# Performance work log

Hardware: AMD Instinct MI355X
Metric: run time of the kernel (lower is better)

The kernel has to match this reference:

```python
import jax, jax.numpy as jnp
import numpy as np

N_NODES = 50000
N_EDGES = 600000
D = 128
THETA = (0.5, -1.0, 0.5)  # len(theta) must be 3 to match learnable_diag[3, in_feats]


def setup_inputs() -> dict:
    key = jax.random.key(0)
    k1, k2, k3, k4, k5 = jax.random.split(key, 5)
    feat = jax.random.normal(k1, (N_NODES, D), dtype=jnp.float32)
    edge_index = jax.random.randint(k2, (2, N_EDGES), 0, N_NODES)  # [src; dst]
    # learnable_diag = torch.rand(3, in_feats)
    diag = jax.random.uniform(k3, (3, D), dtype=jnp.float32)
    # nn.Linear(out_feats, out_feats) with xavier_uniform weight, zero bias
    limit = float(np.sqrt(6.0 / (D + D)))
    W = jax.random.uniform(k4, (D, D), dtype=jnp.float32, minval=-limit, maxval=limit)
    b = jnp.zeros((D,), dtype=jnp.float32)
    return {"feat": feat, "edge_index": edge_index, "diag": diag, "W": W, "b": b}


def reference(feat, edge_index, diag, W, b):
    src, dst = edge_index[0], edge_index[1]
    n = feat.shape[0]
    # in_degrees: count of incoming edges per node
    deg = jax.ops.segment_sum(jnp.ones_like(dst, dtype=feat.dtype), dst, num_segments=n)
    d_invsqrt = jnp.clip(deg, 1.0, None) ** -0.5  # [N]
    d_invsqrt = d_invsqrt[:, None]  # [N,1]

    h = (THETA[0] * feat) * diag[0]
    h = h @ W.T + b  # nn.Linear

    for k in range(1, len(THETA)):
        # unnLaplacian: feat - (A @ (feat * Dinv)) * Dinv * diag[k]
        msg = feat * d_invsqrt  # [N,D]
        agg = jax.ops.segment_sum(msg[src], dst, num_segments=n)  # SpMM: copy_u + sum
        feat = feat - agg * d_invsqrt * diag[k]
        h = h + THETA[k] * feat
    return h
```

## Files before the change

kernel.cpp:

```cpp
#include <hip/hip_runtime.h>

#define NN 50000
#define NE 600000
#define D  128
#define NBLK 196

typedef __attribute__((ext_vector_type(8))) short bf16x8;
typedef __attribute__((ext_vector_type(4))) float floatx4;

__device__ __forceinline__ unsigned short bf16_rne(float f) {
    union { float f; unsigned u; } v; v.f = f;
    unsigned r = v.u + 0x7FFFu + ((v.u >> 16) & 1u);
    return (unsigned short)(r >> 16);
}
__device__ __forceinline__ unsigned pack2(float a, float b) {
    return (unsigned)bf16_rne(a) | ((unsigned)bf16_rne(b) << 16);
}

__global__ __launch_bounds__(256) void prep_kernel(const float* __restrict__ W,
                                                   const float* __restrict__ diag,
                                                   unsigned short* __restrict__ Wb,
                                                   int* __restrict__ deg_i,
                                                   unsigned int* __restrict__ zrow0,
                                                   unsigned int* __restrict__ zrow1) {
    int g = blockIdx.x * 256 + threadIdx.x;
    if (g < NN) deg_i[g] = 0;
    if (g < 16384) {
        int j = g & 127;
        Wb[g] = bf16_rne(0.5f * diag[j] * W[g]);
    }
    if (g < 64) { zrow0[g] = 0u; zrow1[g] = 0u; }
}

__global__ __launch_bounds__(256) void hist_kernel(const int* __restrict__ dst,
                                                   int* __restrict__ deg_i) {
    int e = blockIdx.x * 256 + threadIdx.x;
    if (e < NE) atomicAdd(&deg_i[dst[e]], 1);
}

__global__ __launch_bounds__(256) void scan1_kernel(const int* __restrict__ deg_i,
                                                    int* __restrict__ row_ptr,
                                                    int* __restrict__ partials,
                                                    float* __restrict__ dinvf,
                                                    float* __restrict__ rdegf) {
    __shared__ int sh[256];
    int i = blockIdx.x * 256 + threadIdx.x;
    int dg = (i < NN) ? deg_i[i] : 0;
    if (i < NN) {
        float d = (float)dg;
        float dc = d > 1.0f ? d : 1.0f;
        dinvf[i] = rsqrtf(dc);
        rdegf[i] = sqrtf(dc);
    }
    sh[threadIdx.x] = dg;
    __syncthreads();
    #pragma unroll
    for (int off = 1; off < 256; off <<= 1) {
        int t = (threadIdx.x >= off) ? sh[threadIdx.x - off] : 0;
        __syncthreads();
        sh[threadIdx.x] += t;
        __syncthreads();
    }
    if (i < NN) row_ptr[i + 1] = sh[threadIdx.x];
    if (threadIdx.x == 255) partials[blockIdx.x] = sh[255];
}

__global__ __launch_bounds__(256) void scan2_kernel(int* __restrict__ partials) {
    __shared__ int sh[256];
    sh[threadIdx.x] = (threadIdx.x < NBLK) ? partials[threadIdx.x] : 0;
    __syncthreads();
    #pragma unroll
    for (int off = 1; off < 256; off <<= 1) {
        int t = (threadIdx.x >= off) ? sh[threadIdx.x - off] : 0;
        __syncthreads();
        sh[threadIdx.x] += t;
        __syncthreads();
    }
    if (threadIdx.x < NBLK) partials[threadIdx.x] = sh[threadIdx.x];
}

__global__ __launch_bounds__(256) void scan3_kernel(int* __restrict__ row_ptr,
                                                    const int* __restrict__ partials,
                                                    int* __restrict__ fillc) {
    int i = blockIdx.x * 256 + threadIdx.x;
    if (i < NN) {
        int add = (blockIdx.x > 0) ? partials[blockIdx.x - 1] : 0;
        row_ptr[i + 1] += add;
        fillc[i] = 0;
    }
    if (i == 0) row_ptr[0] = 0;
}

__global__ __launch_bounds__(256) void fill_kernel(const int* __restrict__ src,
                                                   const int* __restrict__ dst,
                                                   const int* __restrict__ row_ptr,
                                                   int* __restrict__ fillc,
                                                   int* __restrict__ csr) {
    int e = blockIdx.x * 256 + threadIdx.x;
    if (e < NE) {
        int t = dst[e];
        int pos = row_ptr[t] + atomicAdd(&fillc[t], 1);
        csr[pos] = src[e];
    }
}

__global__ __launch_bounds__(256) void gemm_mfma_kernel(const float* __restrict__ feat,
                                                        const unsigned short* __restrict__ Wb,
                                                        const float* __restrict__ b,
                                                        const float* __restrict__ dinvf,
                                                        unsigned short* __restrict__ featb_s,
                                                        float* __restrict__ out) {
    const int wv   = threadIdx.x >> 6;
    const int lane = threadIdx.x & 63;
    const int r16  = lane & 15;
    const int quad = lane >> 4;
    const int m0   = blockIdx.x * 64 + wv * 16;

    const int mrow = m0 + r16;
    const int mc   = (mrow < NN) ? mrow : (NN - 1);
    const float* arow = feat + (size_t)mc * D + quad * 8;
    const float di = dinvf[mc];

    bf16x8 afrag[4];
    #pragma unroll
    for (int kc = 0; kc < 4; ++kc) {
        const float4 f0 = *(const float4*)(arow + kc * 32);
        const float4 f1 = *(const float4*)(arow + kc * 32 + 4);
        bf16x8 a;
        a[0] = (short)bf16_rne(f0.x); a[1] = (short)bf16_rne(f0.y);
        a[2] = (short)bf16_rne(f0.z); a[3] = (short)bf16_rne(f0.w);
        a[4] = (short)bf16_rne(f1.x); a[5] = (short)bf16_rne(f1.y);
        a[6] = (short)bf16_rne(f1.z); a[7] = (short)bf16_rne(f1.w);
        afrag[kc] = a;
        if (mrow < NN) {
            uint4 st;
            st.x = pack2(f0.x * di, f0.y * di);
            st.y = pack2(f0.z * di, f0.w * di);
            st.z = pack2(f1.x * di, f1.y * di);
            st.w = pack2(f1.z * di, f1.w * di);
            *(uint4*)(featb_s + (size_t)mc * D + quad * 8 + kc * 32) = st;
        }
    }

    floatx4 acc[8];
    #pragma unroll
    for (int nt = 0; nt < 8; ++nt) acc[nt] = (floatx4)(0.0f);

    #pragma unroll
    for (int nt = 0; nt < 8; ++nt) {
        const unsigned short* brow = Wb + (size_t)(nt * 16 + r16) * D + quad * 8;
        #pragma unroll
        for (int kc = 0; kc < 4; ++kc) {
            const bf16x8 bfrag = *(const bf16x8*)(brow + kc * 32);
            acc[nt] = __builtin_amdgcn_mfma_f32_16x16x32_bf16(afrag[kc], bfrag, acc[nt], 0, 0, 0);
        }
    }

    #pragma unroll
    for (int nt = 0; nt < 8; ++nt) {
        const int d = nt * 16 + r16;
        const float bd = b[d];
        #pragma unroll
        for (int r = 0; r < 4; ++r) {
            const int i = m0 + quad * 4 + r;
            if (i < NN) out[(size_t)i * D + d] = acc[nt][r] + bd;
        }
    }
}

__device__ __forceinline__ float2 gather_acc(const unsigned short* __restrict__ rows,
                                             const int* __restrict__ csr,
                                             int e0, int e1, int lane) {
    float2 acc = make_float2(0.0f, 0.0f);
    for (int bse = e0; bse < e1; bse += 64) {
        int idx = bse + lane;
        int s = (idx < e1) ? csr[idx] : NN;
        int cnt8 = (min(64, e1 - bse) + 7) & ~7;
        for (int k = 0; k < cnt8; k += 8) {
            #pragma unroll
            for (int u = 0; u < 8; ++u) {
                int ss = __shfl(s, k + u);
                unsigned pv = *(const unsigned*)(rows + (size_t)ss * D + 2 * lane);
                acc.x += __uint_as_float(pv << 16);
                acc.y += __uint_as_float(pv & 0xFFFF0000u);
            }
        }
    }
    return acc;
}

__global__ __launch_bounds__(256) void gather1_kernel(const unsigned short* __restrict__ featb_s,
                                                      const int* __restrict__ csr,
                                                      const int* __restrict__ row_ptr,
                                                      const float* __restrict__ dinvf,
                                                      const float* __restrict__ diag,
                                                      const float* __restrict__ feat0,
                                                      unsigned int* __restrict__ feat1s) {
    const int node = blockIdx.x * 4 + (threadIdx.x >> 6);
    const int lane = threadIdx.x & 63;
    float2 acc = gather_acc(featb_s, csr, row_ptr[node], row_ptr[node + 1], lane);

    const size_t o2 = (size_t)node * (D / 2) + lane;
    const float di = dinvf[node];
    const float2 bs = *(const float2*)&feat0[2 * o2];
    const float2 dg = *(const float2*)&diag[D + 2 * lane];
    float rx = bs.x - acc.x * di * dg.x;
    float ry = bs.y - acc.y * di * dg.y;
    feat1s[o2] = pack2(rx * di, ry * di);
}

__global__ __launch_bounds__(256) void gather2_kernel(const unsigned short* __restrict__ feat1s,
                                                      const int* __restrict__ csr,
                                                      const int* __restrict__ row_ptr,
                                                      const float* __restrict__ dinvf,
                                                      const float* __restrict__ rdegf,
                                                      const float* __restrict__ diag,
                                                      float* __restrict__ outp) {
    const int node = blockIdx.x * 4 + (threadIdx.x >> 6);
    const int lane = threadIdx.x & 63;
    float2 acc = gather_acc(feat1s, csr, row_ptr[node], row_ptr[node + 1], lane);

    const size_t o2 = (size_t)node * (D / 2) + lane;
    const float di = dinvf[node];
    const float rd = rdegf[node];
    const unsigned bp = ((const unsigned*)feat1s)[o2];
    const float2 dg = *(const float2*)&diag[2 * D + 2 * lane];
    float bx = __uint_as_float(bp << 16) * rd;
    float by = __uint_as_float(bp & 0xFFFF0000u) * rd;
    float2 cur = *(const float2*)&outp[2 * o2];
    cur.x -= 0.5f * (bx + acc.x * di * dg.x);
    cur.y -= 0.5f * (by + acc.y * di * dg.y);
    *(float2*)&outp[2 * o2] = cur;
}

extern "C" void kernel_launch(void* const* d_in, const int* in_sizes, int n_in,
                              void* d_out, int out_size, void* d_ws, size_t ws_size,
                              hipStream_t stream) {
    const float* feat = (const float*)d_in[0];
    const int*   eidx = (const int*)d_in[1];
    const float* diag = (const float*)d_in[2];
    const float* W    = (const float*)d_in[3];
    const float* b    = (const float*)d_in[4];
    float* out = (float*)d_out;

    const int* src = eidx;
    const int* dst = eidx + NE;

    unsigned short* featb_s = (unsigned short*)d_ws;
    unsigned short* feat1s  = featb_s + (size_t)(NN + 1) * D;
    int*   csr      = (int*)(feat1s + (size_t)(NN + 1) * D);
    float* dinvf    = (float*)(csr + NE);
    float* rdegf    = dinvf + NN;
    int*   deg_i    = (int*)(rdegf + NN);
    int*   row_ptr  = deg_i + NN;
    int*   fillc    = row_ptr + NN + 2;
    int*   partials = fillc + NN;
    unsigned short* Wb = (unsigned short*)(partials + 256);

    prep_kernel<<<NBLK, 256, 0, stream>>>(W, diag, Wb, deg_i,
                                          (unsigned int*)(featb_s + (size_t)NN * D),
                                          (unsigned int*)(feat1s + (size_t)NN * D));

    hist_kernel<<<(NE + 255) / 256, 256, 0, stream>>>(dst, deg_i);
    scan1_kernel<<<NBLK, 256, 0, stream>>>(deg_i, row_ptr, partials, dinvf, rdegf);
    scan2_kernel<<<1, 256, 0, stream>>>(partials);
    scan3_kernel<<<NBLK, 256, 0, stream>>>(row_ptr, partials, fillc);
    fill_kernel<<<(NE + 255) / 256, 256, 0, stream>>>(src, dst, row_ptr, fillc, csr);

    gemm_mfma_kernel<<<(NN + 63) / 64, 256, 0, stream>>>(feat, Wb, b, dinvf, featb_s, out);

    gather1_kernel<<<NN / 4, 256, 0, stream>>>(featb_s, csr, row_ptr, dinvf, diag,
                                               feat, (unsigned int*)feat1s);
    gather2_kernel<<<NN / 4, 256, 0, stream>>>(feat1s, csr, row_ptr, dinvf, rdegf, diag, out);
}
```

Before: 229.4 us.

## Fuse CSR build stages into one cooperative kernel with grid syncs

Merges the prep, histogram, three scan stages and CSR fill into a single cooperative kernel of 784 blocks, with grid-wide syncs between phases. The aim is to cut the launch overhead and inter-kernel gaps of six small launches. In exchange each phase runs on a fixed grid with grid-stride loops. Grid sync barriers carry their own cost and can limit occupancy.

```diff
diff --git a/kernel.cpp b/kernel.cpp
--- a/kernel.cpp
+++ b/kernel.cpp
@@ -1,9 +1,13 @@
 #include <hip/hip_runtime.h>
+#include <hip/hip_cooperative_groups.h>
+
+namespace cg = cooperative_groups;
 
 #define NN 50000
 #define NE 600000
 #define D  128
 #define NBLK 196
+#define CGRID 784
 
 typedef __attribute__((ext_vector_type(8))) short bf16x8;
 typedef __attribute__((ext_vector_type(4))) float floatx4;
@@ -17,89 +21,84 @@
     return (unsigned)bf16_rne(a) | ((unsigned)bf16_rne(b) << 16);
 }
 
-__global__ __launch_bounds__(256) void prep_kernel(const float* __restrict__ W,
-                                                   const float* __restrict__ diag,
-                                                   unsigned short* __restrict__ Wb,
-                                                   int* __restrict__ deg_i,
-                                                   unsigned int* __restrict__ zrow0,
-                                                   unsigned int* __restrict__ zrow1) {
-    int g = blockIdx.x * 256 + threadIdx.x;
+__global__ __launch_bounds__(256) void build_kernel(const int* __restrict__ src,
+                                                    const int* __restrict__ dst,
+                                                    const float* __restrict__ W,
+                                                    const float* __restrict__ diag,
+                                                    unsigned short* __restrict__ Wb,
+                                                    int* __restrict__ deg_i,
+                                                    int* __restrict__ row_ptr,
+                                                    int* __restrict__ fillc,
+                                                    int* __restrict__ partials,
+                                                    float* __restrict__ dinvf,
+                                                    float* __restrict__ rdegf,
+                                                    int* __restrict__ csr,
+                                                    unsigned int* __restrict__ zrow0,
+                                                    unsigned int* __restrict__ zrow1) {
+    cg::grid_group grid = cg::this_grid();
+    __shared__ int sh[256];
+    const int t = threadIdx.x;
+    const int b = blockIdx.x;
+    const int g = b * 256 + t;
+    const int G = CGRID * 256;
+
     if (g < NN) deg_i[g] = 0;
     if (g < 16384) {
         int j = g & 127;
         Wb[g] = bf16_rne(0.5f * diag[j] * W[g]);
     }
     if (g < 64) { zrow0[g] = 0u; zrow1[g] = 0u; }
-}
-
-__global__ __launch_bounds__(256) void hist_kernel(const int* __restrict__ dst,
-                                                   int* __restrict__ deg_i) {
-    int e = blockIdx.x * 256 + threadIdx.x;
-    if (e < NE) atomicAdd(&deg_i[dst[e]], 1);
-}
-
-__global__ __launch_bounds__(256) void scan1_kernel(const int* __restrict__ deg_i,
-                                                    int* __restrict__ row_ptr,
-                                                    int* __restrict__ partials,
-                                                    float* __restrict__ dinvf,
-                                                    float* __restrict__ rdegf) {
-    __shared__ int sh[256];
-    int i = blockIdx.x * 256 + threadIdx.x;
-    int dg = (i < NN) ? deg_i[i] : 0;
-    if (i < NN) {
-        float d = (float)dg;
-        float dc = d > 1.0f ? d : 1.0f;
-        dinvf[i] = rsqrtf(dc);
-        rdegf[i] = sqrtf(dc);
-    }
-    sh[threadIdx.x] = dg;
-    __syncthreads();
-    #pragma unroll
-    for (int off = 1; off < 256; off <<= 1) {
-        int t = (threadIdx.x >= off) ? sh[threadIdx.x - off] : 0;
+    grid.sync();
+
+    for (int e = g; e < NE; e += G) atomicAdd(&deg_i[dst[e]], 1);
+    grid.sync();
+
+    if (b < NBLK) {
+        int i = b * 256 + t;
+        int dg = (i < NN) ? deg_i[i] : 0;
+        if (i < NN) {
+            float d = (float)dg;
+            float dc = d > 1.0f ? d : 1.0f;
+            dinvf[i] = rsqrtf(dc);
+            rdegf[i] = sqrtf(dc);
+        }
+        sh[t] = dg;
         __syncthreads();
-        sh[threadIdx.x] += t;
+        #pragma unroll
+        for (int off = 1; off < 256; off <<= 1) {
+            int v = (t >= off) ? sh[t - off] : 0;
+            __syncthreads();
+            sh[t] += v;
+            __syncthreads();
+        }
+        if (i < NN) row_ptr[i + 1] = sh[t];
+        if (t == 255) partials[b] = sh[255];
+    }
+    grid.sync();
+
+    if (b < NBLK) {
+        sh[t] = (t < NBLK) ? partials[t] : 0;
         __syncthreads();
-    }
-    if (i < NN) row_ptr[i + 1] = sh[threadIdx.x];
-    if (threadIdx.x == 255) partials[blockIdx.x] = sh[255];
-}
-
-__global__ __launch_bounds__(256) void scan2_kernel(int* __restrict__ partials) {
-    __shared__ int sh[256];
-    sh[threadIdx.x] = (threadIdx.x < NBLK) ? partials[threadIdx.x] : 0;
-    __syncthreads();
-    #pragma unroll
-    for (int off = 1; off < 256; off <<= 1) {
-        int t = (threadIdx.x >= off) ? sh[threadIdx.x - off] : 0;
-        __syncthreads();
-        sh[threadIdx.x] += t;
-        __syncthreads();
-    }
-    if (threadIdx.x < NBLK) partials[threadIdx.x] = sh[threadIdx.x];
-}
-
-__global__ __launch_bounds__(256) void scan3_kernel(int* __restrict__ row_ptr,
-                                                    const int* __restrict__ partials,
-                                                    int* __restrict__ fillc) {
-    int i = blockIdx.x * 256 + threadIdx.x;
-    if (i < NN) {
-        int add = (blockIdx.x > 0) ? partials[blockIdx.x - 1] : 0;
-        row_ptr[i + 1] += add;
-        fillc[i] = 0;
-    }
-    if (i == 0) row_ptr[0] = 0;
-}
-
-__global__ __launch_bounds__(256) void fill_kernel(const int* __restrict__ src,
-                                                   const int* __restrict__ dst,
-                                                   const int* __restrict__ row_ptr,
-                                                   int* __restrict__ fillc,
-                                                   int* __restrict__ csr) {
-    int e = blockIdx.x * 256 + threadIdx.x;
-    if (e < NE) {
-        int t = dst[e];
-        int pos = row_ptr[t] + atomicAdd(&fillc[t], 1);
+        #pragma unroll
+        for (int off = 1; off < 256; off <<= 1) {
+            int v = (t >= off) ? sh[t - off] : 0;
+            __syncthreads();
+            sh[t] += v;
+            __syncthreads();
+        }
+        int add = (b > 0) ? sh[b - 1] : 0;
+        int i = b * 256 + t;
+        if (i < NN) {
+            row_ptr[i + 1] += add;
+            fillc[i] = 0;
+        }
+        if (g == 0) row_ptr[0] = 0;
+    }
+    grid.sync();
+
+    for (int e = g; e < NE; e += G) {
+        int tt = dst[e];
+        int pos = row_ptr[tt] + atomicAdd(&fillc[tt], 1);
         csr[pos] = src[e];
     }
 }
@@ -257,15 +256,19 @@
     int*   partials = fillc + NN;
     unsigned short* Wb = (unsigned short*)(partials + 256);
 
-    prep_kernel<<<NBLK, 256, 0, stream>>>(W, diag, Wb, deg_i,
-                                          (unsigned int*)(featb_s + (size_t)NN * D),
-                                          (unsigned int*)(feat1s + (size_t)NN * D));
-
-    hist_kernel<<<(NE + 255) / 256, 256, 0, stream>>>(dst, deg_i);
-    scan1_kernel<<<NBLK, 256, 0, stream>>>(deg_i, row_ptr, partials, dinvf, rdegf);
-    scan2_kernel<<<1, 256, 0, stream>>>(partials);
-    scan3_kernel<<<NBLK, 256, 0, stream>>>(row_ptr, partials, fillc);
-    fill_kernel<<<(NE + 255) / 256, 256, 0, stream>>>(src, dst, row_ptr, fillc, csr);
+    unsigned int* zrow0 = (unsigned int*)(featb_s + (size_t)NN * D);
+    unsigned int* zrow1 = (unsigned int*)(feat1s + (size_t)NN * D);
+
+    {
+        void* args[] = {
+            (void*)&src, (void*)&dst, (void*)&W, (void*)&diag,
+            (void*)&Wb, (void*)&deg_i, (void*)&row_ptr, (void*)&fillc,
+            (void*)&partials, (void*)&dinvf, (void*)&rdegf, (void*)&csr,
+            (void*)&zrow0, (void*)&zrow1
+        };
+        hipLaunchCooperativeKernel((void*)build_kernel, dim3(CGRID), dim3(256),
+                                   args, 0, stream);
+    }
 
     gemm_mfma_kernel<<<(NN + 63) / 64, 256, 0, stream>>>(feat, Wb, b, dinvf, featb_s, out);
 
```

Result: slower. 527.7 us (+130.1%).
